# Kernel optimization log

Hardware: AMD Instinct MI355X
Metric: run time of the kernel (lower is better)

## Reference

```python
import jax, jax.numpy as jnp
import numpy as np

BS, NPTS, NQ, N, E = 8, 4096, 4096, 1024, 8192
F_, D, DY, H, OUT, STEPS = 256, 2, 3, 256, 3, 16


def setup_inputs() -> dict:
    key = jax.random.key(0)
    ks = jax.random.split(key, 12)
    s = 0.05
    return {
        "inp_x": jax.random.uniform(ks[0], (BS, NPTS, D), dtype=jnp.float32),
        "inp_y": jax.random.normal(ks[1], (BS, NPTS, DY), dtype=jnp.float32),
        "q": jax.random.uniform(ks[2], (BS, NQ, D), dtype=jnp.float32),
        "node_pos": jax.random.uniform(ks[3], (N, D), dtype=jnp.float32),
        "W_e1": jax.random.normal(ks[4], (D + DY, H), dtype=jnp.float32) * s,
        "b_e1": jnp.zeros((H,), jnp.float32),
        "W_e2": jax.random.normal(ks[5], (H, F_), dtype=jnp.float32) * s,
        "b_e2": jnp.zeros((F_,), jnp.float32),
        "W_g": jax.random.normal(ks[6], (F_ + D, F_), dtype=jnp.float32) * s,
        "b_g": jnp.zeros((F_,), jnp.float32),
        "ln_g": jnp.ones((F_,), jnp.float32),
        "ln_b": jnp.zeros((F_,), jnp.float32),
        "W_d1": jax.random.normal(ks[7], (F_ + D, H), dtype=jnp.float32) * s,
        "b_d1": jnp.zeros((H,), jnp.float32),
        "W_d2": jax.random.normal(ks[8], (H, OUT), dtype=jnp.float32) * s,
        "b_d2": jnp.zeros((OUT,), jnp.float32),
        "edge_index": jax.random.randint(ks[9], (2, E), 0, N, dtype=jnp.int32),
        "msg_steps": STEPS,
    }


def _mlp(x, W1, b1, W2, b2):
    # 2-layer ReLU MLP (matches repo's NN encoder/decoder structure)
    return jnp.maximum(x @ W1 + b1, 0.0) @ W2 + b2


def _soft_coord(pos, x):
    # GENSoftNN repr_fn: softmax over nodes of -||x - pos||^2.
    # pos [N,D], x [B,P,D] -> [B,P,N]; expand ||x-p||^2 to avoid [B,P,N,D].
    d = (jnp.sum(x * x, -1)[..., None]
         + jnp.sum(pos * pos, -1)[None, None, :]
         - 2.0 * jnp.einsum('bpd,nd->bpn', x, pos))
    return jax.nn.softmax(-d, axis=-1)


def _layer_norm(x, g, b, eps=1e-5):
    m = jnp.mean(x, -1, keepdims=True)
    v = jnp.mean((x - m) ** 2, -1, keepdims=True)  # biased var, torch LN
    return (x - m) * jax.lax.rsqrt(v + eps) * g + b


def reference(inp_x, inp_y, q, node_pos, W_e1, b_e1, W_e2, b_e2, W_g, b_g,
              ln_g, ln_b, W_d1, b_d1, W_d2, b_d2, edge_index, msg_steps):
    n = node_pos.shape[0]
    # --- GCNConv symmetric normalization with self-loops (PyG default) ---
    loops = jnp.arange(n, dtype=edge_index.dtype)
    src = jnp.concatenate([edge_index[0], loops])  # message source (x_j)
    dst = jnp.concatenate([edge_index[1], loops])  # aggregation target
    deg = jnp.zeros((n,), jnp.float32).at[dst].add(1.0)
    dinv = jax.lax.rsqrt(jnp.maximum(deg, 1e-12))
    norm = (dinv[src] * dinv[dst])[None, :, None]  # [1, E+N, 1]

    # --- encode input points and project onto nodes ---
    enc = _mlp(jnp.concatenate([inp_x, inp_y], -1), W_e1, b_e1, W_e2, b_e2)  # [B,P,F]
    inp_coord = _soft_coord(node_pos, inp_x)                                  # [B,P,N]
    x = jnp.einsum('bpn,bpf->bnf', inp_coord, enc)                            # [B,N,F]

    pos_b = jnp.broadcast_to(node_pos[None], (x.shape[0], n, node_pos.shape[1]))

    # --- msg_steps of  LN(x + GCNConv(cat(pos, x))) ---
    def step(x, _):
        h = jnp.concatenate([pos_b, x], -1) @ W_g        # lin first: [B,N,F]
        msg = h[:, src, :] * norm                         # gather + scale
        agg = jnp.zeros_like(h).at[:, dst, :].add(msg) + b_g  # scatter-add
        return _layer_norm(x + agg, ln_g, ln_b), None

    x, _ = jax.lax.scan(step, x, None, length=msg_steps)

    # --- decode queries ---
    q_coord = _soft_coord(node_pos, q)                    # [B,Q,N]
    lat = jnp.einsum('bqn,bnf->bqf', q_coord, x)          # [B,Q,F]
    return _mlp(jnp.concatenate([lat, q], -1), W_d1, b_d1, W_d2, b_d2)
```

## Files before the change

### kernel.cpp

```cpp
#include <hip/hip_runtime.h>

#define BB 8
#define NP 4096
#define NN 1024
#define NE 8192
#define FF 256
#define TS 264
#define NSTEP 16
#define NSEG 64
#define SEGSZ 128

typedef float f32x4_t __attribute__((ext_vector_type(4)));
typedef __bf16 bf16x8_t __attribute__((ext_vector_type(8)));
typedef unsigned int u32x4_t __attribute__((ext_vector_type(4)));
typedef unsigned int u32x2_t __attribute__((ext_vector_type(2)));

static __device__ __forceinline__ unsigned short f2bf(float f) {
  return __builtin_bit_cast(unsigned short, static_cast<__bf16>(f));
}
static __device__ __forceinline__ float ashf(unsigned short s) {
  union { unsigned u; float f; } t; t.u = (unsigned)s << 16; return t.f;
}
static __device__ __forceinline__ void split_pk(float a, float b, unsigned& h, unsigned& l) {
  unsigned short ha = f2bf(a), hb = f2bf(b);
  unsigned short la = f2bf(a - ashf(ha)), lb = f2bf(b - ashf(hb));
  h = (unsigned)ha | ((unsigned)hb << 16);
  l = (unsigned)la | ((unsigned)lb << 16);
}
static __device__ __forceinline__ f32x4_t mfma16(u32x4_t a, u32x4_t b, f32x4_t c) {
  return __builtin_amdgcn_mfma_f32_16x16x32_bf16(
      __builtin_bit_cast(bf16x8_t, a), __builtin_bit_cast(bf16x8_t, b), c, 0, 0, 0);
}
static __device__ __forceinline__ int swz16(int e) { return e ^ ((e >> 3) & 7); }

__global__ __launch_bounds__(1024) void k_cnt(const int* __restrict__ dstA,
                                              int* __restrict__ cntg) {
  __shared__ int ds[SEGSZ];
  int seg = blockIdx.x, n = threadIdx.x;
  if (n < SEGSZ) ds[n] = dstA[seg * SEGSZ + n];
  __syncthreads();
  int c = 0;
  #pragma unroll 8
  for (int e = 0; e < SEGSZ; e++) c += (ds[e] == n) ? 1 : 0;
  cntg[seg * NN + n] = c;
}

__global__ __launch_bounds__(1024) void k_scan2(const int* __restrict__ cntg,
    float* __restrict__ dinv, int* __restrict__ csr_off) {
  __shared__ int s[NN];
  int n = threadIdx.x;
  int c = 1;
  for (int sg = 0; sg < NSEG; sg++) c += cntg[sg * NN + n];
  dinv[n] = rsqrtf((float)c);
  s[n] = c;
  __syncthreads();
  for (int st = 1; st < NN; st <<= 1) {
    int v = (n >= st) ? s[n - st] : 0;
    __syncthreads();
    s[n] += v;
    __syncthreads();
  }
  csr_off[n] = s[n] - c;
  if (n == NN - 1) csr_off[NN] = s[n];
}

__global__ __launch_bounds__(1024) void k_fill2(const int* __restrict__ srcA,
    const int* __restrict__ dstA, const float* __restrict__ dinv,
    const int* __restrict__ csr_off, const int* __restrict__ cntg,
    int* __restrict__ csr_src, float* __restrict__ csr_w) {
  int n = threadIdx.x;
  if (blockIdx.x == NSEG) {
    int pos = csr_off[n + 1] - 1;
    csr_src[pos] = n;
    csr_w[pos] = dinv[n] * dinv[n];
    return;
  }
  __shared__ int ds[SEGSZ], ss[SEGSZ];
  int seg = blockIdx.x;
  if (n < SEGSZ) { ds[n] = dstA[seg * SEGSZ + n]; ss[n] = srcA[seg * SEGSZ + n]; }
  __syncthreads();
  int base = csr_off[n];
  for (int s2 = 0; s2 < seg; s2++) base += cntg[s2 * NN + n];
  float dn = dinv[n];
  for (int e = 0; e < SEGSZ; e++) {
    if (ds[e] == n) {
      int sv = ss[e];
      csr_src[base] = sv;
      csr_w[base] = dinv[sv] * dn;
      base++;
    }
  }
}

__global__ __launch_bounds__(256) void k_spos(const float* __restrict__ npos,
    const int* __restrict__ csr_off, const int* __restrict__ csr_src,
    const float* __restrict__ csr_w, float* __restrict__ spos) {
  int n = blockIdx.x * 256 + threadIdx.x;
  if (n >= NN) return;
  float sx = 0.f, sy = 0.f;
  int e1 = csr_off[n + 1];
  for (int e = csr_off[n]; e < e1; e++) {
    float w = csr_w[e]; int s = csr_src[e];
    sx += w * npos[2 * s]; sy += w * npos[2 * s + 1];
  }
  spos[2 * n] = sx; spos[2 * n + 1] = sy;
}

__global__ __launch_bounds__(256) void k_posb(const float* __restrict__ spos,
    const float* __restrict__ Wg, const float* __restrict__ bg, float* __restrict__ sposW) {
  int n = blockIdx.x, f = threadIdx.x;
  sposW[(size_t)n * FF + f] = spos[2 * n] * Wg[f] + spos[2 * n + 1] * Wg[FF + f] + bg[f];
}

__global__ __launch_bounds__(256) void k_stats(const float* __restrict__ inx,
    const float* __restrict__ qxy, const float* __restrict__ npos,
    float* __restrict__ mI, float* __restrict__ liI,
    float* __restrict__ mQ, float* __restrict__ liQ) {
  const float* xy = blockIdx.y ? qxy : inx;
  float* mOut = blockIdx.y ? mQ : mI;
  float* liOut = blockIdx.y ? liQ : liI;
  int wv = threadIdx.x >> 6, lane = threadIdx.x & 63;
  int pt = blockIdx.x * 4 + wv;
  float px = xy[pt * 2], py = xy[pt * 2 + 1];
  float s[16];
  float m = -1e30f;
  #pragma unroll
  for (int k = 0; k < 16; k++) {
    int n = lane + 64 * k;
    float2 np = ((const float2*)npos)[n];
    float dx = px - np.x, dy = py - np.y;
    float v = -(dx * dx + dy * dy);
    s[k] = v; m = fmaxf(m, v);
  }
  #pragma unroll
  for (int o = 32; o; o >>= 1) m = fmaxf(m, __shfl_xor(m, o));
  float l = 0.f;
  #pragma unroll
  for (int k = 0; k < 16; k++) l += __expf(s[k] - m);
  #pragma unroll
  for (int o = 32; o; o >>= 1) l += __shfl_xor(l, o);
  if (lane == 0) { mOut[pt] = m; liOut[pt] = 1.0f / l; }
}

__global__ __launch_bounds__(256) void k_pack_w(const float* __restrict__ We2,
    const float* __restrict__ Wg, const float* __restrict__ Wd1,
    unsigned short* __restrict__ WTe2h, unsigned short* __restrict__ WTe2l,
    unsigned short* __restrict__ WTgh, unsigned short* __restrict__ WTgl,
    unsigned short* __restrict__ WTd1h, unsigned short* __restrict__ WTd1l) {
  int kc = blockIdx.x, which = blockIdx.y, n = threadIdx.x;
  const float* W = (which == 0) ? We2 : (which == 1) ? (Wg + 2 * FF) : Wd1;
  unsigned short* Dh = (which == 0) ? WTe2h : (which == 1) ? WTgh : WTd1h;
  unsigned short* Dl = (which == 0) ? WTe2l : (which == 1) ? WTgl : WTd1l;
  unsigned hu[16], lu[16];
  #pragma unroll
  for (int i = 0; i < 16; i++) {
    float a = W[(kc * 32 + 2 * i) * FF + n];
    float b = W[(kc * 32 + 2 * i + 1) * FF + n];
    split_pk(a, b, hu[i], lu[i]);
  }
  u32x4_t* dvh = (u32x4_t*)(Dh + ((size_t)kc * 256 + n) * 32);
  u32x4_t* dvl = (u32x4_t*)(Dl + ((size_t)kc * 256 + n) * 32);
  #pragma unroll
  for (int i = 0; i < 4; i++) {
    u32x4_t th = {hu[4 * i], hu[4 * i + 1], hu[4 * i + 2], hu[4 * i + 3]};
    u32x4_t tl = {lu[4 * i], lu[4 * i + 1], lu[4 * i + 2], lu[4 * i + 3]};
    dvh[i] = th; dvl[i] = tl;
  }
}

__global__ __launch_bounds__(256) void k_encoder(const float* __restrict__ inx,
    const float* __restrict__ iny, const float* __restrict__ We1,
    const float* __restrict__ be1, const unsigned short* __restrict__ WTe2h,
    const unsigned short* __restrict__ WTe2l, const float* __restrict__ be2,
    unsigned short* __restrict__ encTh, unsigned short* __restrict__ encTl) {
  __shared__ float xin[32][8];
  __shared__ float h[32][TS];
  __shared__ unsigned short Bh[8192];
  __shared__ unsigned short Bl[8192];
  int tid = threadIdx.x;
  int row0 = blockIdx.x * 32;
  int wv = tid >> 6, L = tid & 63, lhi = L >> 4, llo = L & 15;

  if (tid < 160) {
    int pt = tid / 5, d = tid % 5;
    int r = row0 + pt;
    xin[pt][d] = (d < 2) ? inx[r * 2 + d] : iny[r * 3 + (d - 2)];
  }
  __syncthreads();
  {
    int f = tid;
    float w0 = We1[f], w1 = We1[256 + f], w2 = We1[512 + f], w3 = We1[768 + f], w4 = We1[1024 + f];
    float bb = be1[f];
    #pragma unroll 4
    for (int pt = 0; pt < 32; pt++) {
      float v = bb + xin[pt][0]*w0 + xin[pt][1]*w1 + xin[pt][2]*w2 + xin[pt][3]*w3 + xin[pt][4]*w4;
      h[pt][f] = fmaxf(v, 0.f);
    }
  }

  f32x4_t acc[2][4];
  #pragma unroll
  for (int cb = 0; cb < 4; cb++) {
    float bc = be2[wv * 64 + cb * 16 + llo];
    f32x4_t t = {bc, bc, bc, bc};
    acc[0][cb] = t; acc[1][cb] = t;
  }

  for (int kc = 0; kc < 8; kc++) {
    __syncthreads();
    {
      const u32x4_t* sh = (const u32x4_t*)(WTe2h + (size_t)kc * 8192);
      const u32x4_t* sl = (const u32x4_t*)(WTe2l + (size_t)kc * 8192);
      u32x4_t* dh = (u32x4_t*)Bh;
      u32x4_t* dl = (u32x4_t*)Bl;
      #pragma unroll
      for (int i = 0; i < 4; i++) {
        int e = tid + i * 256;
        int es = swz16(e);
        dh[es] = sh[e]; dl[es] = sl[e];
      }
    }
    __syncthreads();
    int kbase = kc * 32 + lhi * 8;
    u32x4_t a0h, a0l, a1h, a1l;
    {
      float p[8];
      *(f32x4_t*)p = *(const f32x4_t*)&h[llo][kbase];
      *(f32x4_t*)(p + 4) = *(const f32x4_t*)&h[llo][kbase + 4];
      unsigned hw[4], lw[4];
      #pragma unroll
      for (int i = 0; i < 4; i++) split_pk(p[2 * i], p[2 * i + 1], hw[i], lw[i]);
      u32x4_t th = {hw[0], hw[1], hw[2], hw[3]}; a0h = th;
      u32x4_t tl = {lw[0], lw[1], lw[2], lw[3]}; a0l = tl;
    }
    {
      float p[8];
      *(f32x4_t*)p = *(const f32x4_t*)&h[llo + 16][kbase];
      *(f32x4_t*)(p + 4) = *(const f32x4_t*)&h[llo + 16][kbase + 4];
      unsigned hw[4], lw[4];
      #pragma unroll
      for (int i = 0; i < 4; i++) split_pk(p[2 * i], p[2 * i + 1], hw[i], lw[i]);
      u32x4_t th = {hw[0], hw[1], hw[2], hw[3]}; a1h = th;
      u32x4_t tl = {lw[0], lw[1], lw[2], lw[3]}; a1l = tl;
    }
    #pragma unroll
    for (int cb = 0; cb < 4; cb++) {
      int col = wv * 64 + cb * 16 + llo;
      int off = swz16(col * 4 + lhi) * 8;
      u32x4_t bh = *(const u32x4_t*)&Bh[off];
      u32x4_t bl = *(const u32x4_t*)&Bl[off];
      acc[0][cb] = mfma16(a0h, bh, mfma16(a0h, bl, mfma16(a0l, bh, acc[0][cb])));
      acc[1][cb] = mfma16(a1h, bh, mfma16(a1h, bl, mfma16(a1l, bh, acc[1][cb])));
    }
  }
  #pragma unroll
  for (int rb = 0; rb < 2; rb++)
    #pragma unroll
    for (int cb = 0; cb < 4; cb++) {
      int col = wv * 64 + cb * 16 + llo;
      f32x4_t v = acc[rb][cb];
      size_t idx = ((size_t)blockIdx.x * 256 + col) * 32 + rb * 16 + lhi * 4;
      unsigned hw0, lw0, hw1, lw1;
      split_pk(v[0], v[1], hw0, lw0);
      split_pk(v[2], v[3], hw1, lw1);
      u32x2_t wh = {hw0, hw1}; *(u32x2_t*)&encTh[idx] = wh;
      u32x2_t wl = {lw0, lw1}; *(u32x2_t*)&encTl[idx] = wl;
    }
}

__global__ __launch_bounds__(256) void k_proj1(const float* __restrict__ inx,
    const float* __restrict__ mI, const float* __restrict__ liI,
    const float* __restrict__ npos, const unsigned short* __restrict__ encTh,
    const unsigned short* __restrict__ encTl, float* __restrict__ part) {
  __shared__ unsigned short BstH[2][8192];
  __shared__ unsigned short BstL[2][8192];
  __shared__ unsigned short AstH[2][1024];
  __shared__ unsigned short AstL[2][1024];
  int tid = threadIdx.x;
  int id = blockIdx.x;
  int xcd = id & 7, kid = id >> 3;
  int slice = xcd * 4 + (kid >> 5);
  int n0 = (kid & 31) * 32;
  int b = slice >> 2, z = slice & 3;
  int wv = tid >> 6, L = tid & 63, lhi = L >> 4, llo = L & 15;
  int an = tid >> 3, t7 = tid & 7, ap = t7 * 4;
  float2 npv = ((const float2*)npos)[n0 + an];
  int pbase0 = b * NP + z * 1024;
  int aoff = swz16(an * 4 + (t7 >> 1)) * 8 + (t7 & 1) * 4;

  auto stageA = [&](int kc, int buf) {
    int p = pbase0 + kc * 32 + ap;
    float c[4];
    #pragma unroll
    for (int j = 0; j < 4; j++) {
      float2 pxy = ((const float2*)inx)[p + j];
      float mm = mI[p + j], ll = liI[p + j];
      float dx = pxy.x - npv.x, dy = pxy.y - npv.y;
      c[j] = __expf(-(dx * dx + dy * dy) - mm) * ll;
    }
    unsigned hw0, lw0, hw1, lw1;
    split_pk(c[0], c[1], hw0, lw0);
    split_pk(c[2], c[3], hw1, lw1);
    u32x2_t wh = {hw0, hw1}; *(u32x2_t*)&AstH[buf][aoff] = wh;
    u32x2_t wl = {lw0, lw1}; *(u32x2_t*)&AstL[buf][aoff] = wl;
  };
  auto stageB = [&](int kc, int buf) {
    const u32x4_t* sh = (const u32x4_t*)(encTh + (size_t)(b * 128 + z * 32 + kc) * 8192);
    const u32x4_t* sl = (const u32x4_t*)(encTl + (size_t)(b * 128 + z * 32 + kc) * 8192);
    u32x4_t* dh = (u32x4_t*)BstH[buf];
    u32x4_t* dl = (u32x4_t*)BstL[buf];
    #pragma unroll
    for (int i = 0; i < 4; i++) {
      int e = tid + i * 256;
      int es = swz16(e);
      dh[es] = sh[e]; dl[es] = sl[e];
    }
  };

  f32x4_t acc[2][4];
  #pragma unroll
  for (int i = 0; i < 2; i++)
    #pragma unroll
    for (int j = 0; j < 4; j++) { f32x4_t t = {0.f, 0.f, 0.f, 0.f}; acc[i][j] = t; }

  stageA(0, 0); stageB(0, 0);
  __syncthreads();
  int a0off = swz16(llo * 4 + lhi) * 8;
  int a1off = swz16((llo + 16) * 4 + lhi) * 8;
  for (int kc = 0; kc < 32; kc++) {
    int cur = kc & 1;
    if (kc < 31) { stageA(kc + 1, cur ^ 1); stageB(kc + 1, cur ^ 1); }
    u32x4_t a0h = *(const u32x4_t*)&AstH[cur][a0off];
    u32x4_t a0l = *(const u32x4_t*)&AstL[cur][a0off];
    u32x4_t a1h = *(const u32x4_t*)&AstH[cur][a1off];
    u32x4_t a1l = *(const u32x4_t*)&AstL[cur][a1off];
    #pragma unroll
    for (int cb = 0; cb < 4; cb++) {
      int off = swz16((wv * 64 + cb * 16 + llo) * 4 + lhi) * 8;
      u32x4_t bh = *(const u32x4_t*)&BstH[cur][off];
      u32x4_t bl = *(const u32x4_t*)&BstL[cur][off];
      acc[0][cb] = mfma16(a0h, bh, mfma16(a0h, bl, mfma16(a0l, bh, acc[0][cb])));
      acc[1][cb] = mfma16(a1h, bh, mfma16(a1h, bl, mfma16(a1l, bh, acc[1][cb])));
    }
    __syncthreads();
  }
  float* op = part + (((size_t)(z * BB + b)) * NN + n0) * FF;
  #pragma unroll
  for (int rb = 0; rb < 2; rb++)
    #pragma unroll
    for (int cb = 0; cb < 4; cb++) {
      int col = wv * 64 + cb * 16 + llo;
      f32x4_t v = acc[rb][cb];
      #pragma unroll
      for (int r = 0; r < 4; r++) op[(rb * 16 + lhi * 4 + r) * FF + col] = v[r];
    }
}

__global__ __launch_bounds__(256) void k_reduce(const float* __restrict__ part,
                                                float* __restrict__ x) {
  size_t i = ((size_t)blockIdx.x * 256 + threadIdx.x) * 4;
  const size_t S = (size_t)BB * NN * FF;
  f32x4_t a = *(const f32x4_t*)&part[i];
  f32x4_t b = *(const f32x4_t*)&part[S + i];
  f32x4_t c = *(const f32x4_t*)&part[2 * S + i];
  f32x4_t d = *(const f32x4_t*)&part[3 * S + i];
  f32x4_t r = (a + b) + (c + d);
  *(f32x4_t*)&x[i] = r;
}

__global__ __launch_bounds__(512) void k_msg2(const float* __restrict__ x_in,
    float* __restrict__ x_out, const float* __restrict__ sposW,
    const int* __restrict__ coff, const int* __restrict__ csrc,
    const float* __restrict__ csw, const unsigned short* __restrict__ WTgh,
    const unsigned short* __restrict__ WTgl, const float* __restrict__ lng,
    const float* __restrict__ lnb, int last,
    unsigned short* __restrict__ xTh, unsigned short* __restrict__ xTl) {
  __shared__ unsigned Ah[32][132];
  __shared__ unsigned Al[32][132];
  __shared__ unsigned short Bh[8192];
  __shared__ unsigned short Bl[8192];
  __shared__ float redS[32][8];
  __shared__ float redQ[32][8];
  int tid = threadIdx.x;
  int id = blockIdx.x;
  int b = id & 7;
  int nb = id >> 3;
  int n0 = nb * 32;
  int wv = tid >> 6, L = tid & 63, lhi = L >> 4, llo = L & 15;

  {
    int row = tid >> 4, seg = tid & 15;
    int n = n0 + row;
    float g[16];
    #pragma unroll
    for (int i = 0; i < 16; i++) g[i] = 0.f;
    int e0 = coff[n], e1 = coff[n + 1];
    for (int e = e0; e < e1; e++) {
      float w = csw[e];
      int s = csrc[e];
      const f32x4_t* px = (const f32x4_t*)(x_in + ((size_t)b * NN + s) * FF + seg * 16);
      #pragma unroll
      for (int i = 0; i < 4; i++) {
        f32x4_t v = px[i];
        g[4*i]   += w * v[0]; g[4*i+1] += w * v[1];
        g[4*i+2] += w * v[2]; g[4*i+3] += w * v[3];
      }
    }
    #pragma unroll
    for (int i = 0; i < 8; i++) {
      unsigned h, l;
      split_pk(g[2 * i], g[2 * i + 1], h, l);
      Ah[row][seg * 8 + i] = h;
      Al[row][seg * 8 + i] = l;
    }
  }

  f32x4_t acc[2][2];
  #pragma unroll
  for (int i = 0; i < 2; i++)
    #pragma unroll
    for (int j = 0; j < 2; j++) { f32x4_t t = {0.f, 0.f, 0.f, 0.f}; acc[i][j] = t; }

  for (int kc = 0; kc < 8; kc++) {
    __syncthreads();
    {
      const u32x4_t* sh = (const u32x4_t*)(WTgh + (size_t)kc * 8192);
      const u32x4_t* sl = (const u32x4_t*)(WTgl + (size_t)kc * 8192);
      u32x4_t* dh = (u32x4_t*)Bh;
      u32x4_t* dl = (u32x4_t*)Bl;
      #pragma unroll
      for (int i = 0; i < 2; i++) {
        int e = tid + i * 512;
        int es = swz16(e);
        dh[es] = sh[e]; dl[es] = sl[e];
      }
    }
    __syncthreads();
    u32x4_t a0h = *(const u32x4_t*)&Ah[llo][kc * 16 + lhi * 4];
    u32x4_t a0l = *(const u32x4_t*)&Al[llo][kc * 16 + lhi * 4];
    u32x4_t a1h = *(const u32x4_t*)&Ah[llo + 16][kc * 16 + lhi * 4];
    u32x4_t a1l = *(const u32x4_t*)&Al[llo + 16][kc * 16 + lhi * 4];
    #pragma unroll
    for (int cb = 0; cb < 2; cb++) {
      int off = swz16((wv * 32 + cb * 16 + llo) * 4 + lhi) * 8;
      u32x4_t bh = *(const u32x4_t*)&Bh[off];
      u32x4_t bl = *(const u32x4_t*)&Bl[off];
      acc[0][cb] = mfma16(a0h, bh, mfma16(a0h, bl, mfma16(a0l, bh, acc[0][cb])));
      acc[1][cb] = mfma16(a1h, bh, mfma16(a1h, bl, mfma16(a1l, bh, acc[1][cb])));
    }
  }

  #pragma unroll
  for (int rb = 0; rb < 2; rb++)
    #pragma unroll
    for (int cb = 0; cb < 2; cb++) {
      int col = wv * 32 + cb * 16 + llo;
      #pragma unroll
      for (int r = 0; r < 4; r++) {
        int row = rb * 16 + lhi * 4 + r;
        float sw = sposW[(size_t)(n0 + row) * FF + col];
        float xr = x_in[((size_t)b * NN + n0 + row) * FF + col];
        acc[rb][cb][r] += sw + xr;
      }
    }
  float ps[2][4], pq[2][4];
  #pragma unroll
  for (int rb = 0; rb < 2; rb++)
    #pragma unroll
    for (int r = 0; r < 4; r++) {
      float s = 0.f, q = 0.f;
      #pragma unroll
      for (int cb = 0; cb < 2; cb++) { float y = acc[rb][cb][r]; s += y; q += y * y; }
      #pragma unroll
      for (int m = 1; m < 16; m <<= 1) { s += __shfl_xor(s, m); q += __shfl_xor(q, m); }
      ps[rb][r] = s; pq[rb][r] = q;
    }
  if (llo == 0) {
    #pragma unroll
    for (int rb = 0; rb < 2; rb++)
      #pragma unroll
      for (int r = 0; r < 4; r++) {
        int row = rb * 16 + lhi * 4 + r;
        redS[row][wv] = ps[rb][r];
        redQ[row][wv] = pq[rb][r];
      }
  }
  __syncthreads();
  float mrs[2][4][2];
  #pragma unroll
  for (int rb = 0; rb < 2; rb++)
    #pragma unroll
    for (int r = 0; r < 4; r++) {
      int row = rb * 16 + lhi * 4 + r;
      float S = 0.f, Q = 0.f;
      #pragma unroll
      for (int wq = 0; wq < 8; wq++) { S += redS[row][wq]; Q += redQ[row][wq]; }
      float mean = S * (1.f / 256.f);
      float var = Q * (1.f / 256.f) - mean * mean;
      mrs[rb][r][0] = mean;
      mrs[rb][r][1] = rsqrtf(var + 1e-5f);
    }
  #pragma unroll
  for (int cb = 0; cb < 2; cb++) {
    int col = wv * 32 + cb * 16 + llo;
    float gg = lng[col], bb = lnb[col];
    #pragma unroll
    for (int rb = 0; rb < 2; rb++)
      #pragma unroll
      for (int r = 0; r < 4; r++) {
        int row = rb * 16 + lhi * 4 + r;
        float o = (acc[rb][cb][r] - mrs[rb][r][0]) * mrs[rb][r][1] * gg + bb;
        if (!last) {
          x_out[((size_t)b * NN + n0 + row) * FF + col] = o;
        } else {
          size_t idx = (((size_t)b * 32 + nb) * 256 + col) * 32 + row;
          unsigned short hh = f2bf(o);
          xTh[idx] = hh;
          xTl[idx] = f2bf(o - ashf(hh));
        }
      }
  }
}

__global__ __launch_bounds__(256) void k_proj2(const float* __restrict__ qxy,
    const float* __restrict__ mQ, const float* __restrict__ liQ,
    const float* __restrict__ npos, const unsigned short* __restrict__ xTh,
    const unsigned short* __restrict__ xTl, unsigned short* __restrict__ latTh,
    unsigned short* __restrict__ latTl) {
  __shared__ unsigned short BstH[2][8192];
  __shared__ unsigned short BstL[2][8192];
  __shared__ unsigned short AstH[2][1024];
  __shared__ unsigned short AstL[2][1024];
  __shared__ float nps[NN * 2];
  int tid = threadIdx.x;
  int id = blockIdx.x;
  int b = id & 7;
  int q0b = id >> 3;
  int q0 = q0b * 32;
  int bt = b * 128 + q0b;
  int wv = tid >> 6, L = tid & 63, lhi = L >> 4, llo = L & 15;
  int aq = tid >> 3, t7 = tid & 7, an4 = t7 * 4;
  int aoff = swz16(aq * 4 + (t7 >> 1)) * 8 + (t7 & 1) * 4;

  {
    const f32x4_t* s4 = (const f32x4_t*)npos;
    *(f32x4_t*)&nps[tid * 4] = s4[tid];
    *(f32x4_t*)&nps[(tid + 256) * 4] = s4[tid + 256];
  }
  int qg = b * NP + q0 + aq;
  float2 qv = ((const float2*)qxy)[qg];
  float qm = mQ[qg], qli = liQ[qg];
  __syncthreads();

  auto stageA = [&](int kc, int buf) {
    int nb = kc * 32 + an4;
    float c[4];
    #pragma unroll
    for (int j = 0; j < 4; j++) {
      float nx = nps[(nb + j) * 2], ny = nps[(nb + j) * 2 + 1];
      float dx = qv.x - nx, dy = qv.y - ny;
      c[j] = __expf(-(dx * dx + dy * dy) - qm) * qli;
    }
    unsigned hw0, lw0, hw1, lw1;
    split_pk(c[0], c[1], hw0, lw0);
    split_pk(c[2], c[3], hw1, lw1);
    u32x2_t wh = {hw0, hw1}; *(u32x2_t*)&AstH[buf][aoff] = wh;
    u32x2_t wl = {lw0, lw1}; *(u32x2_t*)&AstL[buf][aoff] = wl;
  };
  auto stageB = [&](int kc, int buf) {
    const u32x4_t* sh = (const u32x4_t*)(xTh + (size_t)(b * 32 + kc) * 8192);
    const u32x4_t* sl = (const u32x4_t*)(xTl + (size_t)(b * 32 + kc) * 8192);
    u32x4_t* dh = (u32x4_t*)BstH[buf];
    u32x4_t* dl = (u32x4_t*)BstL[buf];
    #pragma unroll
    for (int i = 0; i < 4; i++) {
      int e = tid + i * 256;
      int es = swz16(e);
      dh[es] = sh[e]; dl[es] = sl[e];
    }
  };

  f32x4_t acc[2][4];
  #pragma unroll
  for (int i = 0; i < 2; i++)
    #pragma unroll
    for (int j = 0; j < 4; j++) { f32x4_t t = {0.f, 0.f, 0.f, 0.f}; acc[i][j] = t; }

  stageA(0, 0); stageB(0, 0);
  __syncthreads();
  int a0off = swz16(llo * 4 + lhi) * 8;
  int a1off = swz16((llo + 16) * 4 + lhi) * 8;
  for (int kc = 0; kc < 32; kc++) {
    int cur = kc & 1;
    if (kc < 31) { stageA(kc + 1, cur ^ 1); stageB(kc + 1, cur ^ 1); }
    u32x4_t a0h = *(const u32x4_t*)&AstH[cur][a0off];
    u32x4_t a0l = *(const u32x4_t*)&AstL[cur][a0off];
    u32x4_t a1h = *(const u32x4_t*)&AstH[cur][a1off];
    u32x4_t a1l = *(const u32x4_t*)&AstL[cur][a1off];
    #pragma unroll
    for (int cb = 0; cb < 4; cb++) {
      int off = swz16((wv * 64 + cb * 16 + llo) * 4 + lhi) * 8;
      u32x4_t bh = *(const u32x4_t*)&BstH[cur][off];
      u32x4_t bl = *(const u32x4_t*)&BstL[cur][off];
      acc[0][cb] = mfma16(a0h, bh, mfma16(a0h, bl, mfma16(a0l, bh, acc[0][cb])));
      acc[1][cb] = mfma16(a1h, bh, mfma16(a1h, bl, mfma16(a1l, bh, acc[1][cb])));
    }
    __syncthreads();
  }
  #pragma unroll
  for (int rb = 0; rb < 2; rb++)
    #pragma unroll
    for (int cb = 0; cb < 4; cb++) {
      int col = wv * 64 + cb * 16 + llo;
      int fc = col >> 5, kk = col & 31;
      f32x4_t v = acc[rb][cb];
      #pragma unroll
      for (int r = 0; r < 4; r++) {
        size_t idx = ((size_t)bt * 8 + fc) * 1024 + (rb * 16 + lhi * 4 + r) * 32 + kk;
        unsigned short hh = f2bf(v[r]);
        latTh[idx] = hh;
        latTl[idx] = f2bf(v[r] - ashf(hh));
      }
    }
}

__global__ __launch_bounds__(256) void k_decoder(const unsigned short* __restrict__ latTh,
    const unsigned short* __restrict__ latTl, const float* __restrict__ qxy,
    const unsigned short* __restrict__ WTd1h, const unsigned short* __restrict__ WTd1l,
    const float* __restrict__ bd1, const float* __restrict__ Wd1,
    const float* __restrict__ Wd2, const float* __restrict__ bd2, float* __restrict__ out) {
  __shared__ unsigned short BstH[2][8192];
  __shared__ unsigned short BstL[2][8192];
  __shared__ unsigned short AstH[2][1024];
  __shared__ unsigned short AstL[2][1024];
  __shared__ float qs[32][2];
  __shared__ float red[4][32][3];
  int tid = threadIdx.x;
  int bt = blockIdx.x;
  int wv = tid >> 6, L = tid & 63, lhi = L >> 4, llo = L & 15;

  auto stageA = [&](int kc, int buf) {
    if (tid < 128)
      ((u32x4_t*)AstH[buf])[swz16(tid)] = ((const u32x4_t*)(latTh + ((size_t)bt * 8 + kc) * 1024))[tid];
    else
      ((u32x4_t*)AstL[buf])[swz16(tid - 128)] = ((const u32x4_t*)(latTl + ((size_t)bt * 8 + kc) * 1024))[tid - 128];
  };
  auto stageB = [&](int kc, int buf) {
    const u32x4_t* sh = (const u32x4_t*)(WTd1h + (size_t)kc * 8192);
    const u32x4_t* sl = (const u32x4_t*)(WTd1l + (size_t)kc * 8192);
    u32x4_t* dh = (u32x4_t*)BstH[buf];
    u32x4_t* dl = (u32x4_t*)BstL[buf];
    #pragma unroll
    for (int i = 0; i < 4; i++) {
      int e = tid + i * 256;
      int es = swz16(e);
      dh[es] = sh[e]; dl[es] = sl[e];
    }
  };

  if (tid < 64) qs[tid >> 1][tid & 1] = qxy[((size_t)bt * 32 + (tid >> 1)) * 2 + (tid & 1)];
  stageA(0, 0); stageB(0, 0);
  __syncthreads();

  f32x4_t acc[2][4];
  #pragma unroll
  for (int cb = 0; cb < 4; cb++) {
    int col = wv * 64 + cb * 16 + llo;
    float wa = Wd1[256 * FF + col], wb = Wd1[257 * FF + col], bc = bd1[col];
    #pragma unroll
    for (int rb = 0; rb < 2; rb++) {
      f32x4_t t;
      #pragma unroll
      for (int r = 0; r < 4; r++) {
        int row = rb * 16 + lhi * 4 + r;
        t[r] = bc + qs[row][0] * wa + qs[row][1] * wb;
      }
      acc[rb][cb] = t;
    }
  }

  int a0off = swz16(llo * 4 + lhi) * 8;
  int a1off = swz16((llo + 16) * 4 + lhi) * 8;
  for (int kc = 0; kc < 8; kc++) {
    int cur = kc & 1;
    if (kc < 7) { stageA(kc + 1, cur ^ 1); stageB(kc + 1, cur ^ 1); }
    u32x4_t a0h = *(const u32x4_t*)&AstH[cur][a0off];
    u32x4_t a0l = *(const u32x4_t*)&AstL[cur][a0off];
    u32x4_t a1h = *(const u32x4_t*)&AstH[cur][a1off];
    u32x4_t a1l = *(const u32x4_t*)&AstL[cur][a1off];
    #pragma unroll
    for (int cb = 0; cb < 4; cb++) {
      int off = swz16((wv * 64 + cb * 16 + llo) * 4 + lhi) * 8;
      u32x4_t bh = *(const u32x4_t*)&BstH[cur][off];
      u32x4_t bl = *(const u32x4_t*)&BstL[cur][off];
      acc[0][cb] = mfma16(a0h, bh, mfma16(a0h, bl, mfma16(a0l, bh, acc[0][cb])));
      acc[1][cb] = mfma16(a1h, bh, mfma16(a1h, bl, mfma16(a1l, bh, acc[1][cb])));
    }
    __syncthreads();
  }

  float po[2][4][3];
  #pragma unroll
  for (int rb = 0; rb < 2; rb++)
    #pragma unroll
    for (int r = 0; r < 4; r++) { po[rb][r][0] = 0.f; po[rb][r][1] = 0.f; po[rb][r][2] = 0.f; }
  #pragma unroll
  for (int rb = 0; rb < 2; rb++)
    #pragma unroll
    for (int cb = 0; cb < 4; cb++) {
      int col = wv * 64 + cb * 16 + llo;
      float w0 = Wd2[col * 3], w1 = Wd2[col * 3 + 1], w2 = Wd2[col * 3 + 2];
      f32x4_t v = acc[rb][cb];
      #pragma unroll
      for (int r = 0; r < 4; r++) {
        float hv = fmaxf(v[r], 0.f);
        po[rb][r][0] += hv * w0; po[rb][r][1] += hv * w1; po[rb][r][2] += hv * w2;
      }
    }
  #pragma unroll
  for (int o = 8; o; o >>= 1)
    #pragma unroll
    for (int rb = 0; rb < 2; rb++)
      #pragma unroll
      for (int r = 0; r < 4; r++) {
        po[rb][r][0] += __shfl_xor(po[rb][r][0], o);
        po[rb][r][1] += __shfl_xor(po[rb][r][1], o);
        po[rb][r][2] += __shfl_xor(po[rb][r][2], o);
      }
  if (llo == 0) {
    #pragma unroll
    for (int rb = 0; rb < 2; rb++)
      #pragma unroll
      for (int r = 0; r < 4; r++) {
        int row = rb * 16 + lhi * 4 + r;
        red[wv][row][0] = po[rb][r][0];
        red[wv][row][1] = po[rb][r][1];
        red[wv][row][2] = po[rb][r][2];
      }
  }
  __syncthreads();
  if (tid < 96) {
    int row = tid / 3, o = tid % 3;
    float s = red[0][row][o] + red[1][row][o] + red[2][row][o] + red[3][row][o] + bd2[o];
    out[((size_t)bt * 32 + row) * 3 + o] = s;
  }
}

extern "C" void kernel_launch(void* const* d_in, const int* in_sizes, int n_in,
                              void* d_out, int out_size, void* d_ws, size_t ws_size,
                              hipStream_t stream) {
  const float* inx = (const float*)d_in[0];
  const float* iny = (const float*)d_in[1];
  const float* qxy = (const float*)d_in[2];
  const float* npos = (const float*)d_in[3];
  const float* We1 = (const float*)d_in[4];
  const float* be1 = (const float*)d_in[5];
  const float* We2 = (const float*)d_in[6];
  const float* be2 = (const float*)d_in[7];
  const float* Wg  = (const float*)d_in[8];
  const float* bg  = (const float*)d_in[9];
  const float* lng = (const float*)d_in[10];
  const float* lnb = (const float*)d_in[11];
  const float* Wd1 = (const float*)d_in[12];
  const float* bd1 = (const float*)d_in[13];
  const float* Wd2 = (const float*)d_in[14];
  const float* bd2 = (const float*)d_in[15];
  const int* eidx  = (const int*)d_in[16];
  float* out = (float*)d_out;

  char* w = (char*)d_ws;
  auto carve = [&](size_t n) { char* p = w; w += (n + 255) & ~(size_t)255; return p; };
  char* encR = carve((size_t)2 * BB * NP * FF * 2);
  unsigned short* encTh = (unsigned short*)encR;
  unsigned short* encTl = (unsigned short*)(encR + (size_t)BB * NP * FF * 2);
  unsigned short* latTh = encTh;
  unsigned short* latTl = encTl;
  float* xA = (float*)carve((size_t)BB * NN * FF * 4);
  float* xB = (float*)carve((size_t)BB * NN * FF * 4);
  unsigned short* xTh = (unsigned short*)carve((size_t)BB * NN * FF * 2);
  unsigned short* xTl = (unsigned short*)carve((size_t)BB * NN * FF * 2);
  float* part = (float*)carve((size_t)4 * BB * NN * FF * 4);
  float* mI   = (float*)carve((size_t)BB * NP * 4);
  float* liI  = (float*)carve((size_t)BB * NP * 4);
  float* mQ   = (float*)carve((size_t)BB * NP * 4);
  float* liQ  = (float*)carve((size_t)BB * NP * 4);
  unsigned short* WTe2h = (unsigned short*)carve((size_t)8 * 256 * 32 * 2);
  unsigned short* WTe2l = (unsigned short*)carve((size_t)8 * 256 * 32 * 2);
  unsigned short* WTgh  = (unsigned short*)carve((size_t)8 * 256 * 32 * 2);
  unsigned short* WTgl  = (unsigned short*)carve((size_t)8 * 256 * 32 * 2);
  unsigned short* WTd1h = (unsigned short*)carve((size_t)8 * 256 * 32 * 2);
  unsigned short* WTd1l = (unsigned short*)carve((size_t)8 * 256 * 32 * 2);
  float* sposW = (float*)carve((size_t)NN * FF * 4);
  float* dinv = (float*)carve(NN * 4);
  float* spos = (float*)carve(NN * 2 * 4);
  float* csw  = (float*)carve((NE + NN) * 4);
  int* coff   = (int*)carve((NN + 1) * 4);
  int* csrc   = (int*)carve((NE + NN) * 4);
  int* cntg   = (int*)carve((size_t)NSEG * NN * 4);

  const int* esrc = eidx;
  const int* edst = eidx + NE;

  k_cnt<<<dim3(NSEG), dim3(1024), 0, stream>>>(edst, cntg);
  k_scan2<<<dim3(1), dim3(1024), 0, stream>>>(cntg, dinv, coff);
  k_fill2<<<dim3(NSEG + 1), dim3(1024), 0, stream>>>(esrc, edst, dinv, coff, cntg, csrc, csw);
  k_spos<<<dim3(4), dim3(256), 0, stream>>>(npos, coff, csrc, csw, spos);
  k_posb<<<dim3(NN), dim3(256), 0, stream>>>(spos, Wg, bg, sposW);
  k_pack_w<<<dim3(8, 3), dim3(256), 0, stream>>>(We2, Wg, Wd1, WTe2h, WTe2l, WTgh, WTgl,
                                                 WTd1h, WTd1l);

  k_stats<<<dim3(BB * NP / 4, 2), dim3(256), 0, stream>>>(inx, qxy, npos, mI, liI, mQ, liQ);
  k_encoder<<<dim3(BB * NP / 32), dim3(256), 0, stream>>>(inx, iny, We1, be1, WTe2h, WTe2l, be2,
                                                          encTh, encTl);
  k_proj1<<<dim3(1024), dim3(256), 0, stream>>>(inx, mI, liI, npos, encTh, encTl, part);
  k_reduce<<<dim3(BB * NN * FF / 1024), dim3(256), 0, stream>>>(part, xA);
  for (int s = 0; s < NSTEP; s++) {
    const float* xi = (s & 1) ? xB : xA;
    float* xo = (s & 1) ? xA : xB;
    k_msg2<<<dim3(256), dim3(512), 0, stream>>>(xi, xo, sposW, coff, csrc, csw,
                                                WTgh, WTgl, lng, lnb,
                                                (s == NSTEP - 1) ? 1 : 0, xTh, xTl);
  }
  k_proj2<<<dim3(1024), dim3(256), 0, stream>>>(qxy, mQ, liQ, npos, xTh, xTl, latTh, latTl);
  k_decoder<<<dim3(BB * NP / 32), dim3(256), 0, stream>>>(latTh, latTl, qxy, WTd1h, WTd1l,
                                                          bd1, Wd1, Wd2, bd2, out);
}
```

Baseline: 598.1 us.

## Prefetch tiles into registers and halve LDS buffers in GEMM kernels

In k_proj1, k_proj2 and k_decoder, the double-buffered LDS staging is replaced by a single LDS buffer. The next tile's global loads and coordinate math now go into registers while the current tile is in MFMA, and are written to LDS after a barrier. Halving LDS use and adding occupancy hints to launch_bounds aims to fit more blocks per CU so latency is hidden. k_msg2 goes the other way: it gains an LDS double buffer with register prefetch of the weight tiles, overlapping the gather phase with the first weight load. The trade-off is more register pressure and an extra barrier per iteration in the single-buffered kernels.

```diff
diff --git a/kernel.cpp b/kernel.cpp
--- a/kernel.cpp
+++ b/kernel.cpp
@@ -268,14 +268,14 @@
     }
 }
 
-__global__ __launch_bounds__(256) void k_proj1(const float* __restrict__ inx,
+__global__ __launch_bounds__(256, 4) void k_proj1(const float* __restrict__ inx,
     const float* __restrict__ mI, const float* __restrict__ liI,
     const float* __restrict__ npos, const unsigned short* __restrict__ encTh,
     const unsigned short* __restrict__ encTl, float* __restrict__ part) {
-  __shared__ unsigned short BstH[2][8192];
-  __shared__ unsigned short BstL[2][8192];
-  __shared__ unsigned short AstH[2][1024];
-  __shared__ unsigned short AstL[2][1024];
+  __shared__ unsigned short BstH[8192];
+  __shared__ unsigned short BstL[8192];
+  __shared__ unsigned short AstH[1024];
+  __shared__ unsigned short AstL[1024];
   int tid = threadIdx.x;
   int id = blockIdx.x;
   int xcd = id & 7, kid = id >> 3;
@@ -288,7 +288,10 @@
   int pbase0 = b * NP + z * 1024;
   int aoff = swz16(an * 4 + (t7 >> 1)) * 8 + (t7 & 1) * 4;
 
-  auto stageA = [&](int kc, int buf) {
+  u32x4_t rbh[4], rbl[4];
+  unsigned ch0, ch1, cl0, cl1;
+
+  auto coordA = [&](int kc) {
     int p = pbase0 + kc * 32 + ap;
     float c[4];
     #pragma unroll
@@ -298,23 +301,14 @@
       float dx = pxy.x - npv.x, dy = pxy.y - npv.y;
       c[j] = __expf(-(dx * dx + dy * dy) - mm) * ll;
     }
-    unsigned hw0, lw0, hw1, lw1;
-    split_pk(c[0], c[1], hw0, lw0);
-    split_pk(c[2], c[3], hw1, lw1);
-    u32x2_t wh = {hw0, hw1}; *(u32x2_t*)&AstH[buf][aoff] = wh;
-    u32x2_t wl = {lw0, lw1}; *(u32x2_t*)&AstL[buf][aoff] = wl;
+    split_pk(c[0], c[1], ch0, cl0);
+    split_pk(c[2], c[3], ch1, cl1);
   };
-  auto stageB = [&](int kc, int buf) {
+  auto loadB = [&](int kc) {
     const u32x4_t* sh = (const u32x4_t*)(encTh + (size_t)(b * 128 + z * 32 + kc) * 8192);
     const u32x4_t* sl = (const u32x4_t*)(encTl + (size_t)(b * 128 + z * 32 + kc) * 8192);
-    u32x4_t* dh = (u32x4_t*)BstH[buf];
-    u32x4_t* dl = (u32x4_t*)BstL[buf];
-    #pragma unroll
-    for (int i = 0; i < 4; i++) {
-      int e = tid + i * 256;
-      int es = swz16(e);
-      dh[es] = sh[e]; dl[es] = sl[e];
-    }
+    #pragma unroll
+    for (int i = 0; i < 4; i++) { rbh[i] = sh[tid + i * 256]; rbl[i] = sl[tid + i * 256]; }
   };
 
   f32x4_t acc[2][4];
@@ -323,26 +317,34 @@
     #pragma unroll
     for (int j = 0; j < 4; j++) { f32x4_t t = {0.f, 0.f, 0.f, 0.f}; acc[i][j] = t; }
 
-  stageA(0, 0); stageB(0, 0);
-  __syncthreads();
+  coordA(0);
+  loadB(0);
   int a0off = swz16(llo * 4 + lhi) * 8;
   int a1off = swz16((llo + 16) * 4 + lhi) * 8;
   for (int kc = 0; kc < 32; kc++) {
-    int cur = kc & 1;
-    if (kc < 31) { stageA(kc + 1, cur ^ 1); stageB(kc + 1, cur ^ 1); }
-    u32x4_t a0h = *(const u32x4_t*)&AstH[cur][a0off];
-    u32x4_t a0l = *(const u32x4_t*)&AstL[cur][a0off];
-    u32x4_t a1h = *(const u32x4_t*)&AstH[cur][a1off];
-    u32x4_t a1l = *(const u32x4_t*)&AstL[cur][a1off];
+    __syncthreads();
+    #pragma unroll
+    for (int i = 0; i < 4; i++) {
+      int es = swz16(tid + i * 256);
+      ((u32x4_t*)BstH)[es] = rbh[i];
+      ((u32x4_t*)BstL)[es] = rbl[i];
+    }
+    { u32x2_t wh = {ch0, ch1}; *(u32x2_t*)&AstH[aoff] = wh; }
+    { u32x2_t wl = {cl0, cl1}; *(u32x2_t*)&AstL[aoff] = wl; }
+    __syncthreads();
+    if (kc < 31) { loadB(kc + 1); coordA(kc + 1); }
+    u32x4_t a0h = *(const u32x4_t*)&AstH[a0off];
+    u32x4_t a0l = *(const u32x4_t*)&AstL[a0off];
+    u32x4_t a1h = *(const u32x4_t*)&AstH[a1off];
+    u32x4_t a1l = *(const u32x4_t*)&AstL[a1off];
     #pragma unroll
     for (int cb = 0; cb < 4; cb++) {
       int off = swz16((wv * 64 + cb * 16 + llo) * 4 + lhi) * 8;
-      u32x4_t bh = *(const u32x4_t*)&BstH[cur][off];
-      u32x4_t bl = *(const u32x4_t*)&BstL[cur][off];
+      u32x4_t bh = *(const u32x4_t*)&BstH[off];
+      u32x4_t bl = *(const u32x4_t*)&BstL[off];
       acc[0][cb] = mfma16(a0h, bh, mfma16(a0h, bl, mfma16(a0l, bh, acc[0][cb])));
       acc[1][cb] = mfma16(a1h, bh, mfma16(a1h, bl, mfma16(a1l, bh, acc[1][cb])));
     }
-    __syncthreads();
   }
   float* op = part + (((size_t)(z * BB + b)) * NN + n0) * FF;
   #pragma unroll
@@ -377,8 +379,8 @@
     unsigned short* __restrict__ xTh, unsigned short* __restrict__ xTl) {
   __shared__ unsigned Ah[32][132];
   __shared__ unsigned Al[32][132];
-  __shared__ unsigned short Bh[8192];
-  __shared__ unsigned short Bl[8192];
+  __shared__ unsigned short Bh[2][8192];
+  __shared__ unsigned short Bl[2][8192];
   __shared__ float redS[32][8];
   __shared__ float redQ[32][8];
   int tid = threadIdx.x;
@@ -388,6 +390,25 @@
   int n0 = nb * 32;
   int wv = tid >> 6, L = tid & 63, lhi = L >> 4, llo = L & 15;
 
+  u32x4_t rbh[2], rbl[2];
+  auto loadB = [&](int kc) {
+    const u32x4_t* sh = (const u32x4_t*)(WTgh + (size_t)kc * 8192);
+    const u32x4_t* sl = (const u32x4_t*)(WTgl + (size_t)kc * 8192);
+    #pragma unroll
+    for (int i = 0; i < 2; i++) { rbh[i] = sh[tid + i * 512]; rbl[i] = sl[tid + i * 512]; }
+  };
+  auto writeB = [&](int buf) {
+    u32x4_t* dh = (u32x4_t*)Bh[buf];
+    u32x4_t* dl = (u32x4_t*)Bl[buf];
+    #pragma unroll
+    for (int i = 0; i < 2; i++) {
+      int es = swz16(tid + i * 512);
+      dh[es] = rbh[i]; dl[es] = rbl[i];
+    }
+  };
+
+  loadB(0);
+
   {
     int row = tid >> 4, seg = tid & 15;
     int n = n0 + row;
@@ -414,6 +435,8 @@
       Al[row][seg * 8 + i] = l;
     }
   }
+  writeB(0);
+  __syncthreads();
 
   f32x4_t acc[2][2];
   #pragma unroll
@@ -422,20 +445,8 @@
     for (int j = 0; j < 2; j++) { f32x4_t t = {0.f, 0.f, 0.f, 0.f}; acc[i][j] = t; }
 
   for (int kc = 0; kc < 8; kc++) {
-    __syncthreads();
-    {
-      const u32x4_t* sh = (const u32x4_t*)(WTgh + (size_t)kc * 8192);
-      const u32x4_t* sl = (const u32x4_t*)(WTgl + (size_t)kc * 8192);
-      u32x4_t* dh = (u32x4_t*)Bh;
-      u32x4_t* dl = (u32x4_t*)Bl;
-      #pragma unroll
-      for (int i = 0; i < 2; i++) {
-        int e = tid + i * 512;
-        int es = swz16(e);
-        dh[es] = sh[e]; dl[es] = sl[e];
-      }
-    }
-    __syncthreads();
+    int cur = kc & 1;
+    if (kc < 7) loadB(kc + 1);
     u32x4_t a0h = *(const u32x4_t*)&Ah[llo][kc * 16 + lhi * 4];
     u32x4_t a0l = *(const u32x4_t*)&Al[llo][kc * 16 + lhi * 4];
     u32x4_t a1h = *(const u32x4_t*)&Ah[llo + 16][kc * 16 + lhi * 4];
@@ -443,11 +454,13 @@
     #pragma unroll
     for (int cb = 0; cb < 2; cb++) {
       int off = swz16((wv * 32 + cb * 16 + llo) * 4 + lhi) * 8;
-      u32x4_t bh = *(const u32x4_t*)&Bh[off];
-      u32x4_t bl = *(const u32x4_t*)&Bl[off];
+      u32x4_t bh = *(const u32x4_t*)&Bh[cur][off];
+      u32x4_t bl = *(const u32x4_t*)&Bl[cur][off];
       acc[0][cb] = mfma16(a0h, bh, mfma16(a0h, bl, mfma16(a0l, bh, acc[0][cb])));
       acc[1][cb] = mfma16(a1h, bh, mfma16(a1h, bl, mfma16(a1l, bh, acc[1][cb])));
     }
+    if (kc < 7) writeB(cur ^ 1);
+    __syncthreads();
   }
 
   #pragma unroll
@@ -522,15 +535,15 @@
   }
 }
 
-__global__ __launch_bounds__(256) void k_proj2(const float* __restrict__ qxy,
+__global__ __launch_bounds__(256, 3) void k_proj2(const float* __restrict__ qxy,
     const float* __restrict__ mQ, const float* __restrict__ liQ,
     const float* __restrict__ npos, const unsigned short* __restrict__ xTh,
     const unsigned short* __restrict__ xTl, unsigned short* __restrict__ latTh,
     unsigned short* __restrict__ latTl) {
-  __shared__ unsigned short BstH[2][8192];
-  __shared__ unsigned short BstL[2][8192];
-  __shared__ unsigned short AstH[2][1024];
-  __shared__ unsigned short AstL[2][1024];
+  __shared__ unsigned short BstH[8192];
+  __shared__ unsigned short BstL[8192];
+  __shared__ unsigned short AstH[1024];
+  __shared__ unsigned short AstL[1024];
   __shared__ float nps[NN * 2];
   int tid = threadIdx.x;
   int id = blockIdx.x;
@@ -552,7 +565,10 @@
   float qm = mQ[qg], qli = liQ[qg];
   __syncthreads();
 
-  auto stageA = [&](int kc, int buf) {
+  u32x4_t rbh[4], rbl[4];
+  unsigned ch0, ch1, cl0, cl1;
+
+  auto coordA = [&](int kc) {
     int nb = kc * 32 + an4;
     float c[4];
     #pragma unroll
@@ -561,23 +577,14 @@
       float dx = qv.x - nx, dy = qv.y - ny;
       c[j] = __expf(-(dx * dx + dy * dy) - qm) * qli;
     }
-    unsigned hw0, lw0, hw1, lw1;
-    split_pk(c[0], c[1], hw0, lw0);
-    split_pk(c[2], c[3], hw1, lw1);
-    u32x2_t wh = {hw0, hw1}; *(u32x2_t*)&AstH[buf][aoff] = wh;
-    u32x2_t wl = {lw0, lw1}; *(u32x2_t*)&AstL[buf][aoff] = wl;
+    split_pk(c[0], c[1], ch0, cl0);
+    split_pk(c[2], c[3], ch1, cl1);
   };
-  auto stageB = [&](int kc, int buf) {
+  auto loadB = [&](int kc) {
     const u32x4_t* sh = (const u32x4_t*)(xTh + (size_t)(b * 32 + kc) * 8192);
     const u32x4_t* sl = (const u32x4_t*)(xTl + (size_t)(b * 32 + kc) * 8192);
-    u32x4_t* dh = (u32x4_t*)BstH[buf];
-    u32x4_t* dl = (u32x4_t*)BstL[buf];
-    #pragma unroll
-    for (int i = 0; i < 4; i++) {
-      int e = tid + i * 256;
-      int es = swz16(e);
-      dh[es] = sh[e]; dl[es] = sl[e];
-    }
+    #pragma unroll
+    for (int i = 0; i < 4; i++) { rbh[i] = sh[tid + i * 256]; rbl[i] = sl[tid + i * 256]; }
   };
 
   f32x4_t acc[2][4];
@@ -586,26 +593,34 @@
     #pragma unroll
     for (int j = 0; j < 4; j++) { f32x4_t t = {0.f, 0.f, 0.f, 0.f}; acc[i][j] = t; }
 
-  stageA(0, 0); stageB(0, 0);
-  __syncthreads();
+  coordA(0);
+  loadB(0);
   int a0off = swz16(llo * 4 + lhi) * 8;
   int a1off = swz16((llo + 16) * 4 + lhi) * 8;
   for (int kc = 0; kc < 32; kc++) {
-    int cur = kc & 1;
-    if (kc < 31) { stageA(kc + 1, cur ^ 1); stageB(kc + 1, cur ^ 1); }
-    u32x4_t a0h = *(const u32x4_t*)&AstH[cur][a0off];
-    u32x4_t a0l = *(const u32x4_t*)&AstL[cur][a0off];
-    u32x4_t a1h = *(const u32x4_t*)&AstH[cur][a1off];
-    u32x4_t a1l = *(const u32x4_t*)&AstL[cur][a1off];
+    __syncthreads();
+    #pragma unroll
+    for (int i = 0; i < 4; i++) {
+      int es = swz16(tid + i * 256);
+      ((u32x4_t*)BstH)[es] = rbh[i];
+      ((u32x4_t*)BstL)[es] = rbl[i];
+    }
+    { u32x2_t wh = {ch0, ch1}; *(u32x2_t*)&AstH[aoff] = wh; }
+    { u32x2_t wl = {cl0, cl1}; *(u32x2_t*)&AstL[aoff] = wl; }
+    __syncthreads();
+    if (kc < 31) { loadB(kc + 1); coordA(kc + 1); }
+    u32x4_t a0h = *(const u32x4_t*)&AstH[a0off];
+    u32x4_t a0l = *(const u32x4_t*)&AstL[a0off];
+    u32x4_t a1h = *(const u32x4_t*)&AstH[a1off];
+    u32x4_t a1l = *(const u32x4_t*)&AstL[a1off];
     #pragma unroll
     for (int cb = 0; cb < 4; cb++) {
       int off = swz16((wv * 64 + cb * 16 + llo) * 4 + lhi) * 8;
-      u32x4_t bh = *(const u32x4_t*)&BstH[cur][off];
-      u32x4_t bl = *(const u32x4_t*)&BstL[cur][off];
+      u32x4_t bh = *(const u32x4_t*)&BstH[off];
+      u32x4_t bl = *(const u32x4_t*)&BstL[off];
       acc[0][cb] = mfma16(a0h, bh, mfma16(a0h, bl, mfma16(a0l, bh, acc[0][cb])));
       acc[1][cb] = mfma16(a1h, bh, mfma16(a1h, bl, mfma16(a1l, bh, acc[1][cb])));
     }
-    __syncthreads();
   }
   #pragma unroll
   for (int rb = 0; rb < 2; rb++)
@@ -624,42 +639,37 @@
     }
 }
 
-__global__ __launch_bounds__(256) void k_decoder(const unsigned short* __restrict__ latTh,
+__global__ __launch_bounds__(256, 4) void k_decoder(const unsigned short* __restrict__ latTh,
     const unsigned short* __restrict__ latTl, const float* __restrict__ qxy,
     const unsigned short* __restrict__ WTd1h, const unsigned short* __restrict__ WTd1l,
     const float* __restrict__ bd1, const float* __restrict__ Wd1,
     const float* __restrict__ Wd2, const float* __restrict__ bd2, float* __restrict__ out) {
-  __shared__ unsigned short BstH[2][8192];
-  __shared__ unsigned short BstL[2][8192];
-  __shared__ unsigned short AstH[2][1024];
-  __shared__ unsigned short AstL[2][1024];
+  __shared__ unsigned short BstH[8192];
+  __shared__ unsigned short BstL[8192];
+  __shared__ unsigned short AstH[1024];
+  __shared__ unsigned short AstL[1024];
   __shared__ float qs[32][2];
   __shared__ float red[4][32][3];
   int tid = threadIdx.x;
   int bt = blockIdx.x;
   int wv = tid >> 6, L = tid & 63, lhi = L >> 4, llo = L & 15;
 
-  auto stageA = [&](int kc, int buf) {
-    if (tid < 128)
-      ((u32x4_t*)AstH[buf])[swz16(tid)] = ((const u32x4_t*)(latTh + ((size_t)bt * 8 + kc) * 1024))[tid];
-    else
-      ((u32x4_t*)AstL[buf])[swz16(tid - 128)] = ((const u32x4_t*)(latTl + ((size_t)bt * 8 + kc) * 1024))[tid - 128];
-  };
-  auto stageB = [&](int kc, int buf) {
+  u32x4_t rbh[4], rbl[4], ra;
+  auto loadB = [&](int kc) {
     const u32x4_t* sh = (const u32x4_t*)(WTd1h + (size_t)kc * 8192);
     const u32x4_t* sl = (const u32x4_t*)(WTd1l + (size_t)kc * 8192);
-    u32x4_t* dh = (u32x4_t*)BstH[buf];
-    u32x4_t* dl = (u32x4_t*)BstL[buf];
-    #pragma unroll
-    for (int i = 0; i < 4; i++) {
-      int e = tid + i * 256;
-      int es = swz16(e);
-      dh[es] = sh[e]; dl[es] = sl[e];
-    }
+    #pragma unroll
+    for (int i = 0; i < 4; i++) { rbh[i] = sh[tid + i * 256]; rbl[i] = sl[tid + i * 256]; }
   };
+  auto loadA = [&](int kc) {
+    if (tid < 128)
+      ra = ((const u32x4_t*)(latTh + ((size_t)bt * 8 + kc) * 1024))[tid];
+    else
+      ra = ((const u32x4_t*)(latTl + ((size_t)bt * 8 + kc) * 1024))[tid - 128];
+  };
 
   if (tid < 64) qs[tid >> 1][tid & 1] = qxy[((size_t)bt * 32 + (tid >> 1)) * 2 + (tid & 1)];
-  stageA(0, 0); stageB(0, 0);
+  loadB(0); loadA(0);
   __syncthreads();
 
   f32x4_t acc[2][4];
@@ -682,21 +692,29 @@
   int a0off = swz16(llo * 4 + lhi) * 8;
   int a1off = swz16((llo + 16) * 4 + lhi) * 8;
   for (int kc = 0; kc < 8; kc++) {
-    int cur = kc & 1;
-    if (kc < 7) { stageA(kc + 1, cur ^ 1); stageB(kc + 1, cur ^ 1); }
-    u32x4_t a0h = *(const u32x4_t*)&AstH[cur][a0off];
-    u32x4_t a0l = *(const u32x4_t*)&AstL[cur][a0off];
-    u32x4_t a1h = *(const u32x4_t*)&AstH[cur][a1off];
-    u32x4_t a1l = *(const u32x4_t*)&AstL[cur][a1off];
+    __syncthreads();
+    #pragma unroll
+    for (int i = 0; i < 4; i++) {
+      int es = swz16(tid + i * 256);
+      ((u32x4_t*)BstH)[es] = rbh[i];
+      ((u32x4_t*)BstL)[es] = rbl[i];
+    }
+    if (tid < 128) ((u32x4_t*)AstH)[swz16(tid)] = ra;
+    else ((u32x4_t*)AstL)[swz16(tid - 128)] = ra;
+    __syncthreads();
+    if (kc < 7) { loadB(kc + 1); loadA(kc + 1); }
+    u32x4_t a0h = *(const u32x4_t*)&AstH[a0off];
+    u32x4_t a0l = *(const u32x4_t*)&AstL[a0off];
+    u32x4_t a1h = *(const u32x4_t*)&AstH[a1off];
+    u32x4_t a1l = *(const u32x4_t*)&AstL[a1off];
     #pragma unroll
     for (int cb = 0; cb < 4; cb++) {
       int off = swz16((wv * 64 + cb * 16 + llo) * 4 + lhi) * 8;
-      u32x4_t bh = *(const u32x4_t*)&BstH[cur][off];
-      u32x4_t bl = *(const u32x4_t*)&BstL[cur][off];
+      u32x4_t bh = *(const u32x4_t*)&BstH[off];
+      u32x4_t bl = *(const u32x4_t*)&BstL[off];
       acc[0][cb] = mfma16(a0h, bh, mfma16(a0h, bl, mfma16(a0l, bh, acc[0][cb])));
       acc[1][cb] = mfma16(a1h, bh, mfma16(a1h, bl, mfma16(a1l, bh, acc[1][cb])));
     }
-    __syncthreads();
   }
 
   float po[2][4][3];
```

Measured after the change: 561.2 us. 1.07x faster.
